# Optimization experiments

Measured on AMD Instinct MI355X. Metric: run time of the kernel, lower is better.

The kernel has to match this reference:

```python
import jax, jax.numpy as jnp
import numpy as np

HIDDEN, KEY_DIM, VALUE_DIM = 1024, 1024, 1024
BATCH, SEQ = 8, 2048


def setup_inputs() -> dict:
    key = jax.random.key(0)
    ks = jax.random.split(key, 9)
    s = lambda fan_in: 1.0 / np.sqrt(fan_in)
    return {
        "y_all": jax.random.normal(ks[0], (BATCH, SEQ, HIDDEN), dtype=jnp.float32),
        # torch nn.Linear weights stored as (in, out) for x @ W + b
        "Wq": jax.random.uniform(ks[1], (HIDDEN, KEY_DIM), jnp.float32, -s(HIDDEN), s(HIDDEN)),
        "bq": jax.random.uniform(ks[2], (KEY_DIM,), jnp.float32, -s(HIDDEN), s(HIDDEN)),
        "Wk": jax.random.uniform(ks[3], (HIDDEN, KEY_DIM), jnp.float32, -s(HIDDEN), s(HIDDEN)),
        "bk": jax.random.uniform(ks[4], (KEY_DIM,), jnp.float32, -s(HIDDEN), s(HIDDEN)),
        "Wv": jax.random.uniform(ks[5], (HIDDEN, VALUE_DIM), jnp.float32, -s(HIDDEN), s(HIDDEN)),
        "bv": jax.random.uniform(ks[6], (VALUE_DIM,), jnp.float32, -s(HIDDEN), s(HIDDEN)),
        "Wo": jax.random.uniform(ks[7], (VALUE_DIM, HIDDEN), jnp.float32, -s(VALUE_DIM), s(VALUE_DIM)),
        "bo": jax.random.uniform(ks[8], (HIDDEN,), jnp.float32, -s(VALUE_DIM), s(VALUE_DIM)),
    }


def reference(y_all, Wq, bq, Wk, bk, Wv, bv, Wo, bo):
    # Original loops over t, each step attending last hidden state to the full
    # prefix. Equivalent to a single causal-masked attention pass.
    B, T, H = y_all.shape
    dk = Wq.shape[1]
    q = (y_all @ Wq + bq) / jnp.sqrt(jnp.asarray(dk, y_all.dtype))  # [B,T,dk]
    k = y_all @ Wk + bk                                              # [B,T,dk]
    v = y_all @ Wv + bv                                              # [B,T,dv]
    scores = jnp.einsum("bid,bjd->bij", q, k)                        # [B,T,T]
    causal = jnp.tril(jnp.ones((T, T), dtype=bool))                  # j <= i
    scores = jnp.where(causal, scores, -jnp.inf)
    weights = jax.nn.softmax(scores, axis=-1)
    ctx = jnp.einsum("bij,bjd->bid", weights, v)                     # [B,T,dv]
    return ctx @ Wo + bo                                             # [B,T,H]
```

## Files before the change

### kernel.cpp

```cpp
#include <hip/hip_runtime.h>

typedef __attribute__((ext_vector_type(8))) __bf16 bf16x8;
typedef __attribute__((ext_vector_type(4))) float f32x4;
typedef __attribute__((ext_vector_type(4))) float f4;

__device__ inline void gload16(const void* g, void* l) {
  __builtin_amdgcn_global_load_lds(
      (const __attribute__((address_space(1))) unsigned int*)g,
      (__attribute__((address_space(3))) unsigned int*)l, 16, 0, 0);
}

__global__ void convert_bf16_k(const float* __restrict__ in, __bf16* __restrict__ out, int n8) {
  int i = blockIdx.x * blockDim.x + threadIdx.x;
  int stride = gridDim.x * blockDim.x;
  for (; i < n8; i += stride) {
    f4 a = ((const f4*)in)[2 * (long long)i];
    f4 b = ((const f4*)in)[2 * (long long)i + 1];
    bf16x8 o;
#pragma unroll
    for (int e = 0; e < 4; e++) { o[e] = (__bf16)a[e]; o[e + 4] = (__bf16)b[e]; }
    ((bf16x8*)out)[i] = o;
  }
}

__global__ void pack_bias_k(const float* __restrict__ bq, const float* __restrict__ bk,
                            const float* __restrict__ bv, float* __restrict__ out) {
  int i = blockIdx.x * 256 + threadIdx.x;
  if (i >= 3072) return;
  const float* src = (i < 1024) ? bq : (i < 2048) ? bk : bv;
  out[i] = src[i & 1023];
}

__global__ void transpose_w_k(const float* __restrict__ W0, const float* __restrict__ W1,
                              const float* __restrict__ W2, const float* __restrict__ W3,
                              __bf16* __restrict__ out) {
  int z = blockIdx.z;
  const float* W = (z == 0) ? W0 : (z == 1) ? W1 : (z == 2) ? W2 : W3;
  __bf16* O = out + (long long)z * 1048576;
  __shared__ float tile[32][33];
  int tx = threadIdx.x, ty = threadIdx.y;
  int n0 = blockIdx.x * 32, k0 = blockIdx.y * 32;
#pragma unroll
  for (int i = 0; i < 4; i++)
    tile[ty + i * 8][tx] = W[(long long)(k0 + ty + i * 8) * 1024 + n0 + tx];
  __syncthreads();
#pragma unroll
  for (int i = 0; i < 4; i++)
    O[(long long)(n0 + ty + i * 8) * 1024 + k0 + tx] = (__bf16)tile[tx][ty + i * 8];
}

__global__ void transpose_v_k(const __bf16* __restrict__ V, __bf16* __restrict__ Vt) {
  int z = blockIdx.z;
  const __bf16* src = V + (long long)z * 2097152;
  __bf16* dst = Vt + (long long)z * 2097152;
  __shared__ __bf16 tile[32][33];
  int tx = threadIdx.x, ty = threadIdx.y;
  int d0 = blockIdx.x * 32, t0 = blockIdx.y * 32;
#pragma unroll
  for (int i = 0; i < 4; i++)
    tile[ty + i * 8][tx] = src[(long long)(t0 + ty + i * 8) * 1024 + d0 + tx];
  __syncthreads();
#pragma unroll
  for (int i = 0; i < 4; i++)
    dst[(long long)(d0 + ty + i * 8) * 2048 + t0 + tx] = tile[tx][ty + i * 8];
}


#define ABUF(P, H) (lds + ((P) * 2 + (H)) * 8192)
#define BBUF(P, H) (lds + 32768 + ((P) * 2 + (H)) * 8192)

#define LOADA(P, MIB)                                                          \
  _Pragma("unroll") for (int mi = 0; mi < 4; mi++)                             \
      _Pragma("unroll") for (int kh = 0; kh < 2; kh++) {                       \
    int row = ((MIB) + mi) * 16 + ln15;                                        \
    int pb = (row * 128 + (kh * 32 + kq * 8) * 2) ^ ((row & 7) << 4);          \
    a[mi][kh] = *(const bf16x8*)((const char*)ABUF(P, wm) + pb);               \
  }

#define LOADB(P, NIB)                                                          \
  _Pragma("unroll") for (int ni = 0; ni < 2; ni++)                             \
      _Pragma("unroll") for (int kh = 0; kh < 2; kh++) {                       \
    int row = brow0 + ((NIB) + ni) * 16 + ln15;                                \
    int pb = (row * 128 + (kh * 32 + kq * 8) * 2) ^ ((row & 7) << 4);          \
    b[(NIB) + ni][kh] = *(const bf16x8*)((const char*)BBUF(P, bh) + pb);       \
  }

#define MFMAQ(MI0, NI0)                                                        \
  _Pragma("unroll") for (int mi = 0; mi < 4; mi++)                             \
      _Pragma("unroll") for (int ni = 0; ni < 2; ni++)                         \
          _Pragma("unroll") for (int kh = 0; kh < 2; kh++)                     \
              acc[(MI0) + mi][(NI0) + ni] =                                    \
      __builtin_amdgcn_mfma_f32_16x16x32_bf16(a[mi][kh], b[(NI0) + ni][kh],    \
                                              acc[(MI0) + mi][(NI0) + ni], 0, 0, 0);

#define FENCE asm volatile("" ::: "memory")

#define BARW                                           \
  FENCE;                                               \
  __builtin_amdgcn_s_barrier();                        \
  FENCE;                                               \
  __builtin_amdgcn_s_setprio(1);

#define ENDP                                           \
  __builtin_amdgcn_s_setprio(0);                       \
  FENCE;                                               \
  __builtin_amdgcn_s_barrier();                        \
  FENCE;

#define ENDPB                                          \
  __builtin_amdgcn_s_setprio(0);                       \
  asm volatile("s_waitcnt vmcnt(4)" ::: "memory");     \
  __builtin_amdgcn_s_barrier();                        \
  FENCE;

template <int OUTF32>
__global__ __launch_bounds__(512, 2) void gemm8(
    const __bf16* __restrict__ A0, int lda, long long sAz,
    const __bf16* __restrict__ B0, int ldb, long long sBz,
    void* __restrict__ C0v, int ldc, long long sCz,
    const float* __restrict__ bias0, int sBiasZ,
    float scale_z0, int k_tiles_base, int k_tiles_per_br, int skip_upper) {
  const int nbx = gridDim.x, nby = gridDim.y;
  int lin = (blockIdx.z * nby + blockIdx.y) * nbx + blockIdx.x;
  const int nwg = nbx * nby * gridDim.z;
  const int cpx = nwg >> 3;
  int swz = (lin & 7) * cpx + (lin >> 3);
  const int br = swz % nbx;
  int tmp = swz / nbx;
  const int bc = tmp % nby;
  const int z = tmp / nby;

  if (skip_upper && bc > br) return;
  const int kt = k_tiles_base + k_tiles_per_br * br;

  __shared__ __align__(16) __bf16 lds[65536];

  const int t = threadIdx.x, w = t >> 6, lane = t & 63;
  const int wm = w >> 2, wn = w & 3;
  const int ln15 = lane & 15, kq = lane >> 4;
  const int bh = wn >> 1, brow0 = (wn & 1) * 64;

  const __bf16* A = A0 + (long long)z * sAz + (long long)br * 256 * lda;
  const __bf16* B = B0 + (long long)z * sBz + (long long)bc * 256 * ldb;

  int r0s[2], c0s[2];
#pragma unroll
  for (int i = 0; i < 2; i++) {
    int o = i * 8192 + t * 16;
    int lo = o ^ (((o >> 7) & 7) << 4);
    r0s[i] = lo >> 7;
    c0s[i] = (lo & 127) >> 1;
  }
  const __bf16 *sA0[2], *sA1[2], *sB0[2], *sB1[2];
#pragma unroll
  for (int i = 0; i < 2; i++) {
    sA0[i] = A + (long long)r0s[i] * lda + c0s[i];
    sA1[i] = A + (long long)(r0s[i] + 128) * lda + c0s[i];
    sB0[i] = B + (long long)r0s[i] * ldb + c0s[i];
    sB1[i] = B + (long long)(r0s[i] + 128) * ldb + c0s[i];
  }

  auto stg = [&](const __bf16* const* src, __bf16* lbase, int ktile) {
    int kc = ktile < kt ? ktile : kt - 1;
#pragma unroll
    for (int i = 0; i < 2; i++)
      gload16(src[i] + kc * 64, lbase + i * 4096 + w * 512);
  };

  f32x4 acc[8][4] = {};
  bf16x8 a[4][2], b[4][2];

  stg(sB0, BBUF(0, 0), 0);
  stg(sB1, BBUF(0, 1), 0);
  stg(sA0, ABUF(0, 0), 0);
  stg(sA1, ABUF(0, 1), 0);
  stg(sB0, BBUF(1, 0), 1);
  stg(sB1, BBUF(1, 1), 1);
  asm volatile("s_waitcnt vmcnt(4)" ::: "memory");
  __builtin_amdgcn_s_barrier();
  FENCE;

  for (int kk = 0; kk < kt; kk += 2) {
    LOADA(0, 0) LOADB(0, 0)
    stg(sA0, ABUF(1, 0), kk + 1);
    BARW MFMAQ(0, 0) ENDP
    LOADB(0, 2)
    stg(sA1, ABUF(1, 1), kk + 1);
    BARW MFMAQ(0, 2) ENDP
    LOADA(0, 4)
    stg(sB0, BBUF(0, 0), kk + 2);
    BARW MFMAQ(4, 2) ENDP
    stg(sB1, BBUF(0, 1), kk + 2);
    BARW MFMAQ(4, 0) ENDPB
    LOADA(1, 0) LOADB(1, 0)
    stg(sA0, ABUF(0, 0), kk + 2);
    BARW MFMAQ(0, 0) ENDP
    LOADB(1, 2)
    stg(sA1, ABUF(0, 1), kk + 2);
    BARW MFMAQ(0, 2) ENDP
    LOADA(1, 4)
    stg(sB0, BBUF(1, 0), kk + 3);
    BARW MFMAQ(4, 2) ENDP
    stg(sB1, BBUF(1, 1), kk + 3);
    BARW MFMAQ(4, 0) ENDPB
  }

  const float scale = (z == 0) ? scale_z0 : 1.0f;
  const float* bias = bias0 ? (bias0 + (long long)z * sBiasZ) : nullptr;
  const int row0 = br * 256 + wm * 128 + kq * 4;
  const int col0 = bc * 256 + wn * 64 + ln15;
#pragma unroll
  for (int mi = 0; mi < 8; mi++) {
#pragma unroll
    for (int ni = 0; ni < 4; ni++) {
      const int rr = row0 + mi * 16;
      const int cc = col0 + ni * 16;
      const float bb = bias ? bias[cc] : 0.0f;
#pragma unroll
      for (int j = 0; j < 4; j++) {
        float v = (acc[mi][ni][j] + bb) * scale;
        long long off = (long long)z * sCz + (long long)(rr + j) * ldc + cc;
        if (OUTF32)
          ((float*)C0v)[off] = v;
        else
          ((__bf16*)C0v)[off] = (__bf16)v;
      }
    }
  }
}

__global__ __launch_bounds__(256) void softmax_rows(__bf16* __restrict__ S) {
  const int row = blockIdx.x;
  const int i = row & 2047;
  __bf16* s = S + (long long)row * 2048;
  const int Lpad = (i + 256) & ~255;
  const int t = threadIdx.x;
  const int j0 = t * 8;
  const int wid = t >> 6, lane = t & 63;
  const bool active = j0 < Lpad;

  float v[8];
  float mymax = -3.0e38f;
  if (active) {
    bf16x8 x = *(const bf16x8*)(s + j0);
#pragma unroll
    for (int e = 0; e < 8; e++) {
      float f = (float)x[e];
      v[e] = ((j0 + e) <= i) ? f : -3.0e38f;
      mymax = fmaxf(mymax, v[e]);
    }
  }
  float mw = mymax;
#pragma unroll
  for (int o = 32; o >= 1; o >>= 1) mw = fmaxf(mw, __shfl_xor(mw, o));
  __shared__ float redm[4];
  __shared__ float reds[4];
  if (lane == 0) redm[wid] = mw;
  __syncthreads();
  const float m = fmaxf(fmaxf(redm[0], redm[1]), fmaxf(redm[2], redm[3]));

  float e8[8];
  float mysum = 0.0f;
  if (active) {
#pragma unroll
    for (int e = 0; e < 8; e++) {
      float ev = ((j0 + e) <= i) ? __expf(v[e] - m) : 0.0f;
      e8[e] = ev;
      mysum += ev;
    }
  } else {
#pragma unroll
    for (int e = 0; e < 8; e++) e8[e] = 0.0f;
  }
  float sw = mysum;
#pragma unroll
  for (int o = 32; o >= 1; o >>= 1) sw += __shfl_xor(sw, o);
  if (lane == 0) reds[wid] = sw;
  __syncthreads();
  const float l = reds[0] + reds[1] + reds[2] + reds[3];
  const float rl = 1.0f / l;
  if (active) {
    bf16x8 o;
#pragma unroll
    for (int e = 0; e < 8; e++) o[e] = (__bf16)(e8[e] * rl);
    *(bf16x8*)(s + j0) = o;
  }
}

extern "C" void kernel_launch(void* const* d_in, const int* in_sizes, int n_in,
                              void* d_out, int out_size, void* d_ws, size_t ws_size,
                              hipStream_t stream) {
  const float* y  = (const float*)d_in[0];
  const float* Wq = (const float*)d_in[1];
  const float* bq = (const float*)d_in[2];
  const float* Wk = (const float*)d_in[3];
  const float* bk = (const float*)d_in[4];
  const float* Wv = (const float*)d_in[5];
  const float* bv = (const float*)d_in[6];
  const float* Wo = (const float*)d_in[7];
  const float* bo = (const float*)d_in[8];

  char* ws = (char*)d_ws;
  __bf16* Xb   = (__bf16*)(ws + 0);
  __bf16* Wt   = (__bf16*)(ws + 33554432);
  float*  bqkv = (float*)(ws + 41943040);
  __bf16* Qb   = (__bf16*)(ws + 41955328);
  __bf16* Kb   = (__bf16*)(ws + 75509760);
  __bf16* Vb   = (__bf16*)(ws + 109064192);
  __bf16* Sb   = (__bf16*)(ws + 142618624);

  if (ws_size < 209727488u) return;

  convert_bf16_k<<<2048, 256, 0, stream>>>(y, Xb, 2097152);
  pack_bias_k<<<12, 256, 0, stream>>>(bq, bk, bv, bqkv);
  transpose_w_k<<<dim3(32, 32, 4), dim3(32, 8), 0, stream>>>(Wq, Wk, Wv, Wo, Wt);

  gemm8<0><<<dim3(64, 4, 3), 512, 0, stream>>>(
      Xb, 1024, 0LL, Wt, 1024, 1048576LL,
      Qb, 1024, 16777216LL, bqkv, 1024, 0.03125f, 16, 0, 0);

  gemm8<0><<<dim3(8, 8, 8), 512, 0, stream>>>(
      Qb, 1024, 2097152LL, Kb, 1024, 2097152LL,
      Sb, 2048, 4194304LL, nullptr, 0, 1.0f, 16, 0, 1);

  transpose_v_k<<<dim3(32, 64, 8), dim3(32, 8), 0, stream>>>(Vb, Kb);

  softmax_rows<<<16384, 256, 0, stream>>>(Sb);

  gemm8<0><<<dim3(8, 4, 8), 512, 0, stream>>>(
      Sb, 2048, 4194304LL, Kb, 2048, 2097152LL,
      Qb, 1024, 2097152LL, nullptr, 0, 1.0f, 4, 4, 0);

  gemm8<1><<<dim3(64, 4, 1), 512, 0, stream>>>(
      Qb, 1024, 0LL, Wt + 3 * 1048576, 1024, 0LL,
      d_out, 1024, 0LL, bo, 0, 1.0f, 16, 0, 0);
}
```

Before: 339.8 us.

## Fuse V transpose into QKV GEMM epilogue and launch only causal score tiles

The QKV projection now runs as one GEMM with a 3072-wide output. Q and K are written interleaved into a 2048-stride buffer, and V is written directly in transposed layout from the epilogue, so the separate transpose_v_k kernel goes away. The score GEMM now launches only the 36 lower-triangular tiles per batch, mapped with a sqrt-based triangular index, instead of launching 64 tiles and exiting early on the upper ones. New block-swizzle modes change the tile order. The transposed V stores are narrow 8-byte scattered writes, which may coalesce poorly.

```diff
diff --git a/kernel.cpp b/kernel.cpp
--- a/kernel.cpp
+++ b/kernel.cpp
@@ -3,6 +3,7 @@
 typedef __attribute__((ext_vector_type(8))) __bf16 bf16x8;
 typedef __attribute__((ext_vector_type(4))) float f32x4;
 typedef __attribute__((ext_vector_type(4))) float f4;
+typedef __attribute__((ext_vector_type(4))) unsigned short ushort4_t;
 
 __device__ inline void gload16(const void* g, void* l) {
   __builtin_amdgcn_global_load_lds(
@@ -49,22 +50,6 @@
     O[(long long)(n0 + ty + i * 8) * 1024 + k0 + tx] = (__bf16)tile[tx][ty + i * 8];
 }
 
-__global__ void transpose_v_k(const __bf16* __restrict__ V, __bf16* __restrict__ Vt) {
-  int z = blockIdx.z;
-  const __bf16* src = V + (long long)z * 2097152;
-  __bf16* dst = Vt + (long long)z * 2097152;
-  __shared__ __bf16 tile[32][33];
-  int tx = threadIdx.x, ty = threadIdx.y;
-  int d0 = blockIdx.x * 32, t0 = blockIdx.y * 32;
-#pragma unroll
-  for (int i = 0; i < 4; i++)
-    tile[ty + i * 8][tx] = src[(long long)(t0 + ty + i * 8) * 1024 + d0 + tx];
-  __syncthreads();
-#pragma unroll
-  for (int i = 0; i < 4; i++)
-    dst[(long long)(d0 + ty + i * 8) * 2048 + t0 + tx] = tile[tx][ty + i * 8];
-}
-
 
 #define ABUF(P, H) (lds + ((P) * 2 + (H)) * 8192)
 #define BBUF(P, H) (lds + 32768 + ((P) * 2 + (H)) * 8192)
@@ -113,24 +98,42 @@
   __builtin_amdgcn_s_barrier();                        \
   FENCE;
 
-template <int OUTF32>
+template <int OUT, int SWZ>
 __global__ __launch_bounds__(512, 2) void gemm8(
     const __bf16* __restrict__ A0, int lda, long long sAz,
     const __bf16* __restrict__ B0, int ldb, long long sBz,
     void* __restrict__ C0v, int ldc, long long sCz,
     const float* __restrict__ bias0, int sBiasZ,
-    float scale_z0, int k_tiles_base, int k_tiles_per_br, int skip_upper) {
-  const int nbx = gridDim.x, nby = gridDim.y;
-  int lin = (blockIdx.z * nby + blockIdx.y) * nbx + blockIdx.x;
-  const int nwg = nbx * nby * gridDim.z;
-  const int cpx = nwg >> 3;
-  int swz = (lin & 7) * cpx + (lin >> 3);
-  const int br = swz % nbx;
-  int tmp = swz / nbx;
-  const int bc = tmp % nby;
-  const int z = tmp / nby;
-
-  if (skip_upper && bc > br) return;
+    float scale_z0, int k_tiles_base, int k_tiles_per_br,
+    __bf16* __restrict__ vt_out) {
+  int br, bc, z;
+  {
+    const int lin = (blockIdx.z * gridDim.y + blockIdx.y) * gridDim.x + blockIdx.x;
+    if (SWZ == 1) {
+      const int q = lin & 7, c = lin >> 3;
+      br = q * 8 + (c & 7);
+      bc = c >> 3;
+      z = 0;
+    } else if (SWZ == 2) {
+      const int q = lin & 7, c = lin >> 3;
+      z = q;
+      int b0 = (int)((sqrtf((float)(8 * c + 1)) - 1.0f) * 0.5f);
+      int c0 = c - ((b0 * (b0 + 1)) >> 1);
+      if (c0 < 0) { b0--; c0 = c - ((b0 * (b0 + 1)) >> 1); }
+      if (c0 > b0) { b0++; c0 = c - ((b0 * (b0 + 1)) >> 1); }
+      br = b0;
+      bc = c0;
+    } else {
+      const int nbx = gridDim.x, nby = gridDim.y;
+      const int nwg = nbx * nby * gridDim.z;
+      const int cpx = nwg >> 3;
+      const int swz = (lin & 7) * cpx + (lin >> 3);
+      br = swz % nbx;
+      const int tmp = swz / nbx;
+      bc = tmp % nby;
+      z = tmp / nby;
+    }
+  }
   const int kt = k_tiles_base + k_tiles_per_br * br;
 
   __shared__ __align__(16) __bf16 lds[65536];
@@ -205,25 +208,54 @@
     BARW MFMAQ(4, 0) ENDPB
   }
 
-  const float scale = (z == 0) ? scale_z0 : 1.0f;
-  const float* bias = bias0 ? (bias0 + (long long)z * sBiasZ) : nullptr;
   const int row0 = br * 256 + wm * 128 + kq * 4;
   const int col0 = bc * 256 + wn * 64 + ln15;
-#pragma unroll
-  for (int mi = 0; mi < 8; mi++) {
-#pragma unroll
-    for (int ni = 0; ni < 4; ni++) {
+  if (OUT == 2) {
+#pragma unroll
+    for (int mi = 0; mi < 8; mi++) {
       const int rr = row0 + mi * 16;
-      const int cc = col0 + ni * 16;
-      const float bb = bias ? bias[cc] : 0.0f;
-#pragma unroll
-      for (int j = 0; j < 4; j++) {
-        float v = (acc[mi][ni][j] + bb) * scale;
-        long long off = (long long)z * sCz + (long long)(rr + j) * ldc + cc;
-        if (OUTF32)
-          ((float*)C0v)[off] = v;
-        else
-          ((__bf16*)C0v)[off] = (__bf16)v;
+#pragma unroll
+      for (int ni = 0; ni < 4; ni++) {
+        const int cc = col0 + ni * 16;
+        const float bb = bias0[cc];
+        if (cc < 2048) {
+          const float s = (cc < 1024) ? scale_z0 : 1.0f;
+#pragma unroll
+          for (int j = 0; j < 4; j++)
+            ((__bf16*)C0v)[(long long)(rr + j) * ldc + cc] =
+                (__bf16)((acc[mi][ni][j] + bb) * s);
+        } else {
+          const int d = cc - 2048, bz = rr >> 11, t0 = rr & 2047;
+          ushort4_t p;
+#pragma unroll
+          for (int j = 0; j < 4; j++) {
+            union { __bf16 h; unsigned short u; } cv;
+            cv.h = (__bf16)(acc[mi][ni][j] + bb);
+            p[j] = cv.u;
+          }
+          *(ushort4_t*)(vt_out + (long long)bz * 2097152 + (long long)d * 2048 + t0) = p;
+        }
+      }
+    }
+  } else {
+    const float scale = (z == 0) ? scale_z0 : 1.0f;
+    const float* bias = bias0 ? (bias0 + (long long)z * sBiasZ) : nullptr;
+#pragma unroll
+    for (int mi = 0; mi < 8; mi++) {
+#pragma unroll
+      for (int ni = 0; ni < 4; ni++) {
+        const int rr = row0 + mi * 16;
+        const int cc = col0 + ni * 16;
+        const float bb = bias ? bias[cc] : 0.0f;
+#pragma unroll
+        for (int j = 0; j < 4; j++) {
+          float v = (acc[mi][ni][j] + bb) * scale;
+          long long off = (long long)z * sCz + (long long)(rr + j) * ldc + cc;
+          if (OUT == 1)
+            ((float*)C0v)[off] = v;
+          else
+            ((__bf16*)C0v)[off] = (__bf16)v;
+        }
       }
     }
   }
@@ -304,10 +336,10 @@
   __bf16* Xb   = (__bf16*)(ws + 0);
   __bf16* Wt   = (__bf16*)(ws + 33554432);
   float*  bqkv = (float*)(ws + 41943040);
-  __bf16* Qb   = (__bf16*)(ws + 41955328);
-  __bf16* Kb   = (__bf16*)(ws + 75509760);
-  __bf16* Vb   = (__bf16*)(ws + 109064192);
+  __bf16* QK   = (__bf16*)(ws + 41955328);
+  __bf16* Vt   = (__bf16*)(ws + 109064192);
   __bf16* Sb   = (__bf16*)(ws + 142618624);
+  __bf16* ctx  = (__bf16*)(ws + 0);
 
   if (ws_size < 209727488u) return;
 
@@ -315,23 +347,21 @@
   pack_bias_k<<<12, 256, 0, stream>>>(bq, bk, bv, bqkv);
   transpose_w_k<<<dim3(32, 32, 4), dim3(32, 8), 0, stream>>>(Wq, Wk, Wv, Wo, Wt);
 
-  gemm8<0><<<dim3(64, 4, 3), 512, 0, stream>>>(
-      Xb, 1024, 0LL, Wt, 1024, 1048576LL,
-      Qb, 1024, 16777216LL, bqkv, 1024, 0.03125f, 16, 0, 0);
-
-  gemm8<0><<<dim3(8, 8, 8), 512, 0, stream>>>(
-      Qb, 1024, 2097152LL, Kb, 1024, 2097152LL,
-      Sb, 2048, 4194304LL, nullptr, 0, 1.0f, 16, 0, 1);
-
-  transpose_v_k<<<dim3(32, 64, 8), dim3(32, 8), 0, stream>>>(Vb, Kb);
+  gemm8<2, 1><<<dim3(64, 12, 1), 512, 0, stream>>>(
+      Xb, 1024, 0LL, Wt, 1024, 0LL,
+      QK, 2048, 0LL, bqkv, 0, 0.03125f, 16, 0, Vt);
+
+  gemm8<0, 2><<<dim3(36, 1, 8), 512, 0, stream>>>(
+      QK, 2048, 4194304LL, QK + 1024, 2048, 4194304LL,
+      Sb, 2048, 4194304LL, nullptr, 0, 1.0f, 16, 0, nullptr);
 
   softmax_rows<<<16384, 256, 0, stream>>>(Sb);
 
-  gemm8<0><<<dim3(8, 4, 8), 512, 0, stream>>>(
-      Sb, 2048, 4194304LL, Kb, 2048, 2097152LL,
-      Qb, 1024, 2097152LL, nullptr, 0, 1.0f, 4, 4, 0);
-
-  gemm8<1><<<dim3(64, 4, 1), 512, 0, stream>>>(
-      Qb, 1024, 0LL, Wt + 3 * 1048576, 1024, 0LL,
-      d_out, 1024, 0LL, bo, 0, 1.0f, 16, 0, 0);
-}
+  gemm8<0, 0><<<dim3(8, 4, 8), 512, 0, stream>>>(
+      Sb, 2048, 4194304LL, Vt, 2048, 2097152LL,
+      ctx, 1024, 2097152LL, nullptr, 0, 1.0f, 4, 4, nullptr);
+
+  gemm8<1, 1><<<dim3(64, 4, 1), 512, 0, stream>>>(
+      ctx, 1024, 0LL, Wt + 3 * 1048576, 1024, 0LL,
+      d_out, 1024, 0LL, bo, 0, 1.0f, 16, 0, nullptr);
+}
```

After: 317.3 us. 1.07x faster.
